# Kernel tuning notes

Hardware: AMD Instinct MI355X
Metric: run time of the kernel (lower is better)

Reference implementation:

```python
import jax, jax.numpy as jnp
import numpy as np

B, NA, OB, SD, H, GD = 512, 8, 160, 256, 4, 64
KD = GD + 1   # key_dim = gnn_output_dim + 1 = 65
NU = 32       # Multihead_Attention num_units
ED = 32       # mixing_embed_dim


def _build_edge_index():
    # fully-connected (no self loops) graph per sample, block-diagonal over batch
    idx = np.arange(NA)
    s, d = np.meshgrid(idx, idx, indexing='ij')
    mask = s != d
    s, d = s[mask], d[mask]
    offs = (np.arange(B) * NA)[:, None]
    src = (s[None, :] + offs).reshape(-1)
    dst = (d[None, :] + offs).reshape(-1)
    return jnp.asarray(np.stack([src, dst]), dtype=jnp.int32)


def setup_inputs() -> dict:
    key = jax.random.key(0)
    ks = jax.random.split(key, 16)
    p = lambda i, shape, sc=0.05: jax.random.normal(ks[i], shape, jnp.float32) * sc
    return dict(
        agent_qs=p(0, (B, NA), 1.0),
        obs=p(1, (B, NA, OB), 1.0),
        states=p(2, (B, SD), 1.0),
        edge_index=_build_edge_index(),
        W_gnn=p(3, (OB, GD)), b_gnn=jnp.zeros((GD,), jnp.float32),
        a_src=p(4, (H, GD)), a_dst=p(5, (H, GD)),
        W_h=p(6, (OB, KD * KD)), b_h=jnp.zeros((KD * KD,), jnp.float32),
        Wq=p(7, (SD, NU)), Wk=p(8, (KD, NU)),
        Wv1=p(9, (SD, ED)), bv1=jnp.zeros((ED,), jnp.float32),
        Wv2=p(10, (ED, 1)), bv2=jnp.zeros((1,), jnp.float32),
        Ww1=p(11, (SD, 64)), bw1=jnp.zeros((64,), jnp.float32),
        Ww2=p(12, (64, H)), bw2=jnp.zeros((H,), jnp.float32),
    )


def reference(agent_qs, obs, states, edge_index, W_gnn, b_gnn, a_src, a_dst,
              W_h, b_h, Wq, Wk, Wv1, bv1, Wv2, bv2, Ww1, bw1, Ww2, bw2):
    N = B * NA
    # ---- GraphPyG: GAT-style message passing with per-head edge weights ----
    x = obs.reshape(N, OB)
    h = x @ W_gnn + b_gnn                                        # [N, GD]
    src, dst = edge_index[0], edge_index[1]
    e = jax.nn.leaky_relu(h[src] @ a_src.T + h[dst] @ a_dst.T, 0.2)  # [E, H]
    m = jax.ops.segment_max(e, dst, num_segments=N)              # per-dst softmax
    ex = jnp.exp(e - m[dst])
    s = jax.ops.segment_sum(ex, dst, num_segments=N)
    alpha = ex / (s[dst] + 1e-16)                                # [E, H]
    msg = alpha[:, :, None] * h[src][:, None, :]                 # [E, H, GD]
    agg = jax.ops.segment_sum(msg, dst, num_segments=N).mean(axis=1)
    gcn = jax.nn.relu(agg).reshape(B, NA, GD)

    # ---- COO -> dense per-head weight matrices, diagonal zeroed ----
    dense = jnp.zeros((N, N, H), jnp.float32).at[src, dst].set(alpha)
    diag = jnp.arange(N)
    gnn_weight_matrics = dense.at[diag, diag].set(0.0)           # [N, N, H]

    # ---- hypernet-weighted keys (qgraph_fix branch) ----
    keys = jnp.concatenate([agent_qs[:, :, None], gcn], axis=-1)  # [B, NA, KD]
    w1 = jnp.abs(obs.reshape(-1, OB) @ W_h + b_h).reshape(-1, KD, KD)
    keys = jax.nn.elu(jnp.einsum('nk,nkj->nj', keys.reshape(-1, KD), w1))
    keys = keys.reshape(B, NA, KD)

    # ---- multihead attention mixer: query=state, key=keys, value=agent_qs ----
    d = NU // H
    q = (states @ Wq).reshape(B, 1, H, d).transpose(0, 2, 1, 3)   # [B,H,1,d]
    k = (keys @ Wk).reshape(B, NA, H, d).transpose(0, 2, 1, 3)    # [B,H,NA,d]
    scores = jnp.einsum('bhqd,bhkd->bhqk', q, k) / jnp.sqrt(jnp.float32(d))
    attn = jax.nn.softmax(scores, axis=-1)                        # [B,H,1,NA]
    out = jnp.einsum('bhqk,bk->bhq', attn, agent_qs).transpose(0, 2, 1)  # [B,1,H]

    # ---- squared head weights + state bias V ----
    head_w = (jax.nn.relu(states @ Ww1 + bw1) @ Ww2 + bw2) ** 2   # [B,H]
    q_tot = jnp.sum(out * head_w[:, None, :], axis=-1, keepdims=True)  # [B,1,1]
    v = (jax.nn.relu(states @ Wv1 + bv1) @ Wv2 + bv2)[:, :, None]      # [B,1,1]
    return (q_tot + v, attn, gnn_weight_matrics)
```

## Files before the change

### kernel.cpp

```cpp
#include <hip/hip_runtime.h>


typedef short short8v __attribute__((ext_vector_type(8)));
typedef float float4v __attribute__((ext_vector_type(4)));

#define NBATCH 512
#define NAG 8
#define OBD 160
#define SDD 256
#define NHD 4
#define GDD 64
#define NKD 65
#define NCOL 4225
#define NNODE 4096
#define NSPLIT 8
#define CPS 529
#define OUT1_OFF 512
#define OUT2_OFF 16896
#define DENSE_N4 16777216
#define NFILL 2048
#define NPREP 660
#define NZERO 260
#define WHT_BYTE_OFF 2129920
#define WS_NEED_BF16 3481984

__device__ __forceinline__ ushort f2b(float f) {
    union { float f; uint i; } x; x.f = f;
    uint r = (x.i + 0x7FFFu + ((x.i >> 16) & 1u)) >> 16;
    return (ushort)r;
}

__global__ __launch_bounds__(256) void k_pre(
    const float* __restrict__ aq, const float* __restrict__ obs,
    const float* __restrict__ Wg, const float* __restrict__ bg,
    const float* __restrict__ asrc, const float* __restrict__ adst,
    const float* __restrict__ Wh,
    float* __restrict__ kv, float* __restrict__ keys_acc,
    ushort* __restrict__ WhT, float* __restrict__ dense, int do_prep)
{
    int blk = blockIdx.x, t = threadIdx.x;

    if (blk >= NBATCH) {
        int r = blk - NBATCH;
        if (r < NPREP) {
            if (!do_prep) return;
            for (int i = r * 256 + t; i < NCOL * OBD; i += NPREP * 256) {
                int k = i / NCOL, c = i - k * NCOL;
                WhT[(size_t)c * OBD + k] = f2b(Wh[i]);
            }
        } else {
            int z4 = (r - NPREP) * 256 + t;
            ((float4v*)keys_acc)[z4] = float4v{0.f, 0.f, 0.f, 0.f};
        }
        return;
    }

    int b = blk;
    __shared__ float obs_s[NAG][OBD];
    __shared__ float h_s[NAG][GDD];
    __shared__ float u_s[NAG][NHD], v_s[NAG][NHD];
    __shared__ float al_s[NAG][NAG][NHD];
    __shared__ float c_s[NAG][NAG];

    const float* ob = obs + (size_t)b * (NAG * OBD);
    for (int u = t; u < NAG * OBD; u += 256) obs_s[u / OBD][u % OBD] = ob[u];
    __syncthreads();

    {
        int g = t & 63, i0 = t >> 6;
        float a0 = bg[g], a1 = a0;
        for (int c = 0; c < OBD; ++c) {
            float w = Wg[c * GDD + g];
            a0 += obs_s[i0][c] * w;
            a1 += obs_s[i0 + 4][c] * w;
        }
        h_s[i0][g] = a0; h_s[i0 + 4][g] = a1;
    }
    __syncthreads();

    if (t < 64) {
        int i = (t >> 2) & 7, hd = t & 3;
        const float* av = (t >= 32) ? adst : asrc;
        float a = 0.f;
        for (int g = 0; g < GDD; ++g) a += h_s[i][g] * av[hd * GDD + g];
        if (t >= 32) v_s[i][hd] = a; else u_s[i][hd] = a;
    }
    __syncthreads();

    if (t < 32) {
        int d = t >> 2, hd = t & 3;
        float e[NAG], m = -1e30f;
        for (int s = 0; s < NAG; ++s) {
            if (s == d) { e[s] = -1e30f; continue; }
            float x = u_s[s][hd] + v_s[d][hd];
            x = x > 0.f ? x : 0.2f * x;
            e[s] = x; if (x > m) m = x;
        }
        float sum = 0.f;
        for (int s = 0; s < NAG; ++s) {
            float ex = (s == d) ? 0.f : expf(e[s] - m);
            sum += ex; al_s[s][d][hd] = ex;
        }
        float inv = 1.f / (sum + 1e-16f);
        for (int s = 0; s < NAG; ++s) al_s[s][d][hd] *= inv;
    }
    __syncthreads();

    if (t < 64) {
        int s = t >> 3, d = t & 7;
        c_s[s][d] = 0.25f * (al_s[s][d][0] + al_s[s][d][1] + al_s[s][d][2] + al_s[s][d][3]);
    }
    __syncthreads();

    {
        int g = t & 63, d0 = t >> 6;
        for (int dd = d0; dd < NAG; dd += 4) {
            float a = 0.f;
            for (int s = 0; s < NAG; ++s) a += c_s[s][dd] * h_s[s][g];
            a = a > 0.f ? a : 0.f;
            kv[(size_t)(b * NAG + dd) * NKD + 1 + g] = a;
        }
    }
    if (t < NAG) kv[(size_t)(b * NAG + t) * NKD] = aq[b * NAG + t];

    {
        int s = t >> 5, pos = t & 31, d = pos >> 2, hd = pos & 3;
        float v = (d == s) ? 0.f : al_s[s][d][hd];
        dense[(size_t)(b * NAG + s) * (NNODE * NHD) + b * 32 + pos] = v;
    }
}

__global__ __launch_bounds__(256) void k_fuse_bf16(
    const float* __restrict__ obs, const ushort* __restrict__ WhT,
    const float* __restrict__ bh, const float* __restrict__ kv,
    float* __restrict__ keys_acc, float* __restrict__ dense)
{
    __shared__ float kv_s[64][NKD];
    __shared__ float ak[64][NKD];
    int t = threadIdx.x;

    if (blockIdx.x >= NSPLIT * 64) {
        int fb = blockIdx.x - NSPLIT * 64;
        size_t i = (size_t)fb * 256 + t;
        const size_t stride = (size_t)NFILL * 256;
        float4v z = {0.f, 0.f, 0.f, 0.f};
        float4v* d4 = (float4v*)dense;
        for (; i < DENSE_N4; i += stride) {
            uint off4 = (uint)i & 4095u;
            uint span4 = ((uint)(i >> 15)) << 3;
            if (off4 - span4 < 8u) continue;
            d4[i] = z;
        }
        return;
    }

    int hid = blockIdx.x;
    int ns = hid & 7, mb = hid >> 3;
    int lane = t & 63, w = t >> 6;
    int q = lane >> 4, col = lane & 15;
    int cstart = ns * CPS;
    int cend = NCOL < cstart + CPS ? NCOL : cstart + CPS;

    for (int u = t; u < 64 * NKD; u += 256) {
        ((float*)kv_s)[u] = kv[(size_t)(mb * 64) * NKD + u];
        ((float*)ak)[u] = 0.f;
    }

    int row_g = mb * 64 + w * 16 + col;
    short8v a8[5];
    #pragma unroll
    for (int ks = 0; ks < 5; ++ks) {
        const float* p = obs + (size_t)row_g * OBD + ks * 32 + q * 8;
        float4v lo = *(const float4v*)p;
        float4v hi = *(const float4v*)(p + 4);
        a8[ks] = short8v{(short)f2b(lo[0]), (short)f2b(lo[1]), (short)f2b(lo[2]), (short)f2b(lo[3]),
                         (short)f2b(hi[0]), (short)f2b(hi[1]), (short)f2b(hi[2]), (short)f2b(hi[3])};
    }
    __syncthreads();

    for (int cb = cstart; cb < cend; cb += 16) {
        int c2 = cb + col;
        uint cc = (uint)(c2 < NCOL ? c2 : NCOL - 1);
        float4v acc = {0.f, 0.f, 0.f, 0.f};
        const ushort* bp = WhT + (size_t)cc * OBD;
        #pragma unroll
        for (int ks = 0; ks < 5; ++ks) {
            short8v b8 = *(const short8v*)(bp + ks * 32 + q * 8);
            acc = __builtin_amdgcn_mfma_f32_16x16x32_bf16(a8[ks], b8, acc, 0, 0, 0);
        }
        if (c2 < cend) {
            float bias = bh[c2];
            int k2 = c2 / NKD, j = c2 - k2 * NKD;
            #pragma unroll
            for (int r = 0; r < 4; ++r) {
                int rl = w * 16 + q * 4 + r;
                ak[rl][j] += kv_s[rl][k2] * fabsf(acc[r] + bias);
            }
        }
    }
    __syncthreads();

    for (int u = t; u < 64 * NKD; u += 256)
        atomicAdd(&keys_acc[(size_t)(mb * 64) * NKD + u], ((float*)ak)[u]);
}

__global__ __launch_bounds__(256) void k_fuse_f32(
    const float* __restrict__ obs, const float* __restrict__ Wh,
    const float* __restrict__ bh, const float* __restrict__ kv,
    float* __restrict__ keys_acc, float* __restrict__ dense)
{
    __shared__ float kv_s[64][NKD];
    __shared__ float ak[64][NKD];
    int t = threadIdx.x;

    if (blockIdx.x >= NSPLIT * 64) {
        int fb = blockIdx.x - NSPLIT * 64;
        size_t i = (size_t)fb * 256 + t;
        const size_t stride = (size_t)NFILL * 256;
        float4v z = {0.f, 0.f, 0.f, 0.f};
        float4v* d4 = (float4v*)dense;
        for (; i < DENSE_N4; i += stride) {
            uint off4 = (uint)i & 4095u;
            uint span4 = ((uint)(i >> 15)) << 3;
            if (off4 - span4 < 8u) continue;
            d4[i] = z;
        }
        return;
    }

    int hid = blockIdx.x;
    int ns = hid & 7, mb = hid >> 3;
    int lane = t & 63, w = t >> 6;
    int q = lane >> 4, col = lane & 15;
    int cstart = ns * CPS;
    int cend = NCOL < cstart + CPS ? NCOL : cstart + CPS;

    for (int u = t; u < 64 * NKD; u += 256) {
        ((float*)kv_s)[u] = kv[(size_t)(mb * 64) * NKD + u];
        ((float*)ak)[u] = 0.f;
    }

    int row_g = mb * 64 + w * 16 + col;
    short8v a8[5];
    #pragma unroll
    for (int ks = 0; ks < 5; ++ks) {
        const float* p = obs + (size_t)row_g * OBD + ks * 32 + q * 8;
        float4v lo = *(const float4v*)p;
        float4v hi = *(const float4v*)(p + 4);
        a8[ks] = short8v{(short)f2b(lo[0]), (short)f2b(lo[1]), (short)f2b(lo[2]), (short)f2b(lo[3]),
                         (short)f2b(hi[0]), (short)f2b(hi[1]), (short)f2b(hi[2]), (short)f2b(hi[3])};
    }
    __syncthreads();

    for (int cb = cstart; cb < cend; cb += 16) {
        int c2 = cb + col;
        uint cc = (uint)(c2 < NCOL ? c2 : NCOL - 1);
        float4v acc = {0.f, 0.f, 0.f, 0.f};
        #pragma unroll
        for (int ks = 0; ks < 5; ++ks) {
            uint kbase = (uint)(ks * 32 + q * 8) * (uint)NCOL + cc;
            short8v b8;
            #pragma unroll
            for (int r = 0; r < 8; ++r)
                b8[r] = (short)f2b(Wh[kbase + (uint)r * (uint)NCOL]);
            acc = __builtin_amdgcn_mfma_f32_16x16x32_bf16(a8[ks], b8, acc, 0, 0, 0);
        }
        if (c2 < cend) {
            float bias = bh[c2];
            int k2 = c2 / NKD, j = c2 - k2 * NKD;
            #pragma unroll
            for (int r = 0; r < 4; ++r) {
                int rl = w * 16 + q * 4 + r;
                ak[rl][j] += kv_s[rl][k2] * fabsf(acc[r] + bias);
            }
        }
    }
    __syncthreads();

    for (int u = t; u < 64 * NKD; u += 256)
        atomicAdd(&keys_acc[(size_t)(mb * 64) * NKD + u], ((float*)ak)[u]);
}

__global__ __launch_bounds__(256) void k_attn(
    const float* __restrict__ aq, const float* __restrict__ states,
    const float* __restrict__ keys_acc,
    const float* __restrict__ Wq, const float* __restrict__ Wk,
    const float* __restrict__ Wv1, const float* __restrict__ bv1,
    const float* __restrict__ Wv2, const float* __restrict__ bv2,
    const float* __restrict__ Ww1, const float* __restrict__ bw1,
    const float* __restrict__ Ww2, const float* __restrict__ bw2,
    float* __restrict__ out)
{
    int b = blockIdx.x, t = threadIdx.x;
    __shared__ float st_s[SDD];
    __shared__ float keys_s[NAG][NKD];
    __shared__ float q_s[32], h1_s[64], hv_s[32];
    __shared__ float kp_s[NAG][32];
    __shared__ float oh_s[NHD], hw_s[NHD];

    st_s[t] = states[(size_t)b * SDD + t];
    for (int u = t; u < NAG * NKD; u += 256) {
        int n = u / NKD, j = u - NKD * n;
        float s = keys_acc[(size_t)(b * NAG + n) * NKD + j];
        keys_s[n][j] = s > 0.f ? s : (expf(s) - 1.f);
    }
    __syncthreads();

    if (t < 32) {
        float a = 0.f;
        for (int c = 0; c < SDD; ++c) a += st_s[c] * Wq[c * 32 + t];
        q_s[t] = a;
    } else if (t < 96) {
        int z = t - 32; float a = bw1[z];
        for (int c = 0; c < SDD; ++c) a += st_s[c] * Ww1[c * 64 + z];
        h1_s[z] = fmaxf(a, 0.f);
    } else if (t < 128) {
        int z = t - 96; float a = bv1[z];
        for (int c = 0; c < SDD; ++c) a += st_s[c] * Wv1[c * 32 + z];
        hv_s[z] = fmaxf(a, 0.f);
    }
    __syncthreads();

    {
        int i = t >> 5, u = t & 31;
        float a = 0.f;
        for (int j = 0; j < NKD; ++j) a += keys_s[i][j] * Wk[j * 32 + u];
        kp_s[i][u] = a;
    }
    __syncthreads();

    if (t < NHD) {
        int hd = t;
        float sc[NAG], m = -1e30f;
        for (int i = 0; i < NAG; ++i) {
            float a = 0.f;
            for (int dd = 0; dd < 8; ++dd) a += q_s[hd * 8 + dd] * kp_s[i][hd * 8 + dd];
            a *= 0.35355339059327373f;
            sc[i] = a; if (a > m) m = a;
        }
        float sum = 0.f;
        for (int i = 0; i < NAG; ++i) { sc[i] = expf(sc[i] - m); sum += sc[i]; }
        float inv = 1.f / sum, oh = 0.f;
        for (int i = 0; i < NAG; ++i) {
            float at = sc[i] * inv;
            out[OUT1_OFF + (size_t)(b * NHD + hd) * NAG + i] = at;
            oh += at * aq[b * NAG + i];
        }
        oh_s[hd] = oh;
        float hw = bw2[hd];
        for (int z = 0; z < 64; ++z) hw += h1_s[z] * Ww2[z * NHD + hd];
        hw_s[hd] = hw * hw;
    }
    __syncthreads();

    if (t == 0) {
        float v = bv2[0];
        for (int z = 0; z < 32; ++z) v += hv_s[z] * Wv2[z];
        float qt = 0.f;
        for (int hd = 0; hd < NHD; ++hd) qt += oh_s[hd] * hw_s[hd];
        out[b] = qt + v;
    }
}

extern "C" void kernel_launch(void* const* d_in, const int* in_sizes, int n_in,
                              void* d_out, int out_size, void* d_ws, size_t ws_size,
                              hipStream_t stream) {
    const float* aq   = (const float*)d_in[0];
    const float* obs  = (const float*)d_in[1];
    const float* st   = (const float*)d_in[2];
    const float* Wg   = (const float*)d_in[4];
    const float* bg   = (const float*)d_in[5];
    const float* asrc = (const float*)d_in[6];
    const float* adst = (const float*)d_in[7];
    const float* Wh   = (const float*)d_in[8];
    const float* bh   = (const float*)d_in[9];
    const float* Wq_  = (const float*)d_in[10];
    const float* Wk_  = (const float*)d_in[11];
    const float* Wv1  = (const float*)d_in[12];
    const float* bv1  = (const float*)d_in[13];
    const float* Wv2  = (const float*)d_in[14];
    const float* bv2  = (const float*)d_in[15];
    const float* Ww1  = (const float*)d_in[16];
    const float* bw1  = (const float*)d_in[17];
    const float* Ww2  = (const float*)d_in[18];
    const float* bw2  = (const float*)d_in[19];
    float* out = (float*)d_out;
    float* dense = out + OUT2_OFF;

    float*  kv       = (float*)d_ws;
    float*  keys_acc = kv + (size_t)NNODE * NKD;
    ushort* WhT      = (ushort*)((char*)d_ws + WHT_BYTE_OFF);
    int bf16path = (ws_size >= (size_t)WS_NEED_BF16) ? 1 : 0;

    k_pre<<<NBATCH + NPREP + NZERO, 256, 0, stream>>>(
        aq, obs, Wg, bg, asrc, adst, Wh, kv, keys_acc, WhT, dense, bf16path);

    if (bf16path)
        k_fuse_bf16<<<NSPLIT * 64 + NFILL, 256, 0, stream>>>(obs, WhT, bh, kv, keys_acc, dense);
    else
        k_fuse_f32<<<NSPLIT * 64 + NFILL, 256, 0, stream>>>(obs, Wh, bh, kv, keys_acc, dense);

    k_attn<<<NBATCH, 256, 0, stream>>>(aq, st, keys_acc, Wq_, Wk_, Wv1, bv1, Wv2, bv2,
                                       Ww1, bw1, Ww2, bw2, out);
}
```

Baseline: 115.1 us.

## Reuse B fragments across four row tiles and write per-split partial sums

```diff
diff --git a/kernel.cpp b/kernel.cpp
--- a/kernel.cpp
+++ b/kernel.cpp
@@ -21,8 +21,7 @@
 #define NFILL 2048
 #define NPREP 660
 #define NZERO 260
-#define WHT_BYTE_OFF 2129920
-#define WS_NEED_BF16 3481984
+#define KVN ((size_t)NNODE * NKD)
 
 __device__ __forceinline__ ushort f2b(float f) {
     union { float f; uint i; } x; x.f = f;
@@ -35,7 +34,7 @@
     const float* __restrict__ Wg, const float* __restrict__ bg,
     const float* __restrict__ asrc, const float* __restrict__ adst,
     const float* __restrict__ Wh,
-    float* __restrict__ kv, float* __restrict__ keys_acc,
+    float* __restrict__ kv, float* __restrict__ zptr,
     ushort* __restrict__ WhT, float* __restrict__ dense, int do_prep)
 {
     int blk = blockIdx.x, t = threadIdx.x;
@@ -50,7 +49,7 @@
             }
         } else {
             int z4 = (r - NPREP) * 256 + t;
-            ((float4v*)keys_acc)[z4] = float4v{0.f, 0.f, 0.f, 0.f};
+            ((float4v*)zptr)[z4] = float4v{0.f, 0.f, 0.f, 0.f};
         }
         return;
     }
@@ -130,13 +129,13 @@
     }
 }
 
-__global__ __launch_bounds__(256) void k_fuse_bf16(
-    const float* __restrict__ obs, const ushort* __restrict__ WhT,
-    const float* __restrict__ bh, const float* __restrict__ kv,
-    float* __restrict__ keys_acc, float* __restrict__ dense)
+template<int MODE>
+__global__ __launch_bounds__(256) void k_fuse(
+    const float* __restrict__ obs, const float* __restrict__ Wh,
+    const ushort* __restrict__ WhT, const float* __restrict__ bh,
+    const float* __restrict__ kv, float* __restrict__ outacc,
+    float* __restrict__ dense)
 {
-    __shared__ float kv_s[64][NKD];
-    __shared__ float ak[64][NKD];
     int t = threadIdx.x;
 
     if (blockIdx.x >= NSPLIT * 64) {
@@ -154,8 +153,10 @@
         return;
     }
 
-    int hid = blockIdx.x;
-    int ns = hid & 7, mb = hid >> 3;
+    __shared__ float kv_s[64][NKD];
+    __shared__ float ak[64][NKD];
+
+    int ns = blockIdx.x & 7, mb = blockIdx.x >> 3;
     int lane = t & 63, w = t >> 6;
     int q = lane >> 4, col = lane & 15;
     int cstart = ns * CPS;
@@ -166,124 +167,74 @@
         ((float*)ak)[u] = 0.f;
     }
 
-    int row_g = mb * 64 + w * 16 + col;
-    short8v a8[5];
+    short8v a8[4][5];
     #pragma unroll
-    for (int ks = 0; ks < 5; ++ks) {
-        const float* p = obs + (size_t)row_g * OBD + ks * 32 + q * 8;
-        float4v lo = *(const float4v*)p;
-        float4v hi = *(const float4v*)(p + 4);
-        a8[ks] = short8v{(short)f2b(lo[0]), (short)f2b(lo[1]), (short)f2b(lo[2]), (short)f2b(lo[3]),
-                         (short)f2b(hi[0]), (short)f2b(hi[1]), (short)f2b(hi[2]), (short)f2b(hi[3])};
-    }
-    __syncthreads();
-
-    for (int cb = cstart; cb < cend; cb += 16) {
+    for (int rt = 0; rt < 4; ++rt) {
+        int row_g = mb * 64 + rt * 16 + col;
+        #pragma unroll
+        for (int ks = 0; ks < 5; ++ks) {
+            const float* p = obs + (size_t)row_g * OBD + ks * 32 + q * 8;
+            float4v lo = *(const float4v*)p;
+            float4v hi = *(const float4v*)(p + 4);
+            a8[rt][ks] = short8v{(short)f2b(lo[0]), (short)f2b(lo[1]), (short)f2b(lo[2]), (short)f2b(lo[3]),
+                                 (short)f2b(hi[0]), (short)f2b(hi[1]), (short)f2b(hi[2]), (short)f2b(hi[3])};
+        }
+    }
+    __syncthreads();
+
+    for (int cb = cstart + w * 16; cb < cend; cb += 64) {
         int c2 = cb + col;
         uint cc = (uint)(c2 < NCOL ? c2 : NCOL - 1);
-        float4v acc = {0.f, 0.f, 0.f, 0.f};
-        const ushort* bp = WhT + (size_t)cc * OBD;
+        short8v b8[5];
+        if (MODE == 2) {
+            #pragma unroll
+            for (int ks = 0; ks < 5; ++ks) {
+                uint kbase = (uint)(ks * 32 + q * 8) * (uint)NCOL + cc;
+                #pragma unroll
+                for (int r = 0; r < 8; ++r)
+                    b8[ks][r] = (short)f2b(Wh[kbase + (uint)r * (uint)NCOL]);
+            }
+        } else {
+            const ushort* bp = WhT + (size_t)cc * OBD;
+            #pragma unroll
+            for (int ks = 0; ks < 5; ++ks)
+                b8[ks] = *(const short8v*)(bp + ks * 32 + q * 8);
+        }
+        float4v acc0 = {0,0,0,0}, acc1 = {0,0,0,0}, acc2 = {0,0,0,0}, acc3 = {0,0,0,0};
         #pragma unroll
         for (int ks = 0; ks < 5; ++ks) {
-            short8v b8 = *(const short8v*)(bp + ks * 32 + q * 8);
-            acc = __builtin_amdgcn_mfma_f32_16x16x32_bf16(a8[ks], b8, acc, 0, 0, 0);
+            acc0 = __builtin_amdgcn_mfma_f32_16x16x32_bf16(a8[0][ks], b8[ks], acc0, 0, 0, 0);
+            acc1 = __builtin_amdgcn_mfma_f32_16x16x32_bf16(a8[1][ks], b8[ks], acc1, 0, 0, 0);
+            acc2 = __builtin_amdgcn_mfma_f32_16x16x32_bf16(a8[2][ks], b8[ks], acc2, 0, 0, 0);
+            acc3 = __builtin_amdgcn_mfma_f32_16x16x32_bf16(a8[3][ks], b8[ks], acc3, 0, 0, 0);
         }
         if (c2 < cend) {
             float bias = bh[c2];
             int k2 = c2 / NKD, j = c2 - k2 * NKD;
             #pragma unroll
             for (int r = 0; r < 4; ++r) {
-                int rl = w * 16 + q * 4 + r;
-                ak[rl][j] += kv_s[rl][k2] * fabsf(acc[r] + bias);
+                int rb = q * 4 + r;
+                atomicAdd(&ak[rb     ][j], kv_s[rb     ][k2] * fabsf(acc0[r] + bias));
+                atomicAdd(&ak[rb + 16][j], kv_s[rb + 16][k2] * fabsf(acc1[r] + bias));
+                atomicAdd(&ak[rb + 32][j], kv_s[rb + 32][k2] * fabsf(acc2[r] + bias));
+                atomicAdd(&ak[rb + 48][j], kv_s[rb + 48][k2] * fabsf(acc3[r] + bias));
             }
         }
     }
     __syncthreads();
 
-    for (int u = t; u < 64 * NKD; u += 256)
-        atomicAdd(&keys_acc[(size_t)(mb * 64) * NKD + u], ((float*)ak)[u]);
-}
-
-__global__ __launch_bounds__(256) void k_fuse_f32(
-    const float* __restrict__ obs, const float* __restrict__ Wh,
-    const float* __restrict__ bh, const float* __restrict__ kv,
-    float* __restrict__ keys_acc, float* __restrict__ dense)
-{
-    __shared__ float kv_s[64][NKD];
-    __shared__ float ak[64][NKD];
-    int t = threadIdx.x;
-
-    if (blockIdx.x >= NSPLIT * 64) {
-        int fb = blockIdx.x - NSPLIT * 64;
-        size_t i = (size_t)fb * 256 + t;
-        const size_t stride = (size_t)NFILL * 256;
-        float4v z = {0.f, 0.f, 0.f, 0.f};
-        float4v* d4 = (float4v*)dense;
-        for (; i < DENSE_N4; i += stride) {
-            uint off4 = (uint)i & 4095u;
-            uint span4 = ((uint)(i >> 15)) << 3;
-            if (off4 - span4 < 8u) continue;
-            d4[i] = z;
-        }
-        return;
-    }
-
-    int hid = blockIdx.x;
-    int ns = hid & 7, mb = hid >> 3;
-    int lane = t & 63, w = t >> 6;
-    int q = lane >> 4, col = lane & 15;
-    int cstart = ns * CPS;
-    int cend = NCOL < cstart + CPS ? NCOL : cstart + CPS;
-
-    for (int u = t; u < 64 * NKD; u += 256) {
-        ((float*)kv_s)[u] = kv[(size_t)(mb * 64) * NKD + u];
-        ((float*)ak)[u] = 0.f;
-    }
-
-    int row_g = mb * 64 + w * 16 + col;
-    short8v a8[5];
-    #pragma unroll
-    for (int ks = 0; ks < 5; ++ks) {
-        const float* p = obs + (size_t)row_g * OBD + ks * 32 + q * 8;
-        float4v lo = *(const float4v*)p;
-        float4v hi = *(const float4v*)(p + 4);
-        a8[ks] = short8v{(short)f2b(lo[0]), (short)f2b(lo[1]), (short)f2b(lo[2]), (short)f2b(lo[3]),
-                         (short)f2b(hi[0]), (short)f2b(hi[1]), (short)f2b(hi[2]), (short)f2b(hi[3])};
-    }
-    __syncthreads();
-
-    for (int cb = cstart; cb < cend; cb += 16) {
-        int c2 = cb + col;
-        uint cc = (uint)(c2 < NCOL ? c2 : NCOL - 1);
-        float4v acc = {0.f, 0.f, 0.f, 0.f};
-        #pragma unroll
-        for (int ks = 0; ks < 5; ++ks) {
-            uint kbase = (uint)(ks * 32 + q * 8) * (uint)NCOL + cc;
-            short8v b8;
-            #pragma unroll
-            for (int r = 0; r < 8; ++r)
-                b8[r] = (short)f2b(Wh[kbase + (uint)r * (uint)NCOL]);
-            acc = __builtin_amdgcn_mfma_f32_16x16x32_bf16(a8[ks], b8, acc, 0, 0, 0);
-        }
-        if (c2 < cend) {
-            float bias = bh[c2];
-            int k2 = c2 / NKD, j = c2 - k2 * NKD;
-            #pragma unroll
-            for (int r = 0; r < 4; ++r) {
-                int rl = w * 16 + q * 4 + r;
-                ak[rl][j] += kv_s[rl][k2] * fabsf(acc[r] + bias);
-            }
-        }
-    }
-    __syncthreads();
-
-    for (int u = t; u < 64 * NKD; u += 256)
-        atomicAdd(&keys_acc[(size_t)(mb * 64) * NKD + u], ((float*)ak)[u]);
+    if (MODE == 0) {
+        float* dst = outacc + ((size_t)ns * NNODE + mb * 64) * NKD;
+        for (int u = t; u < 64 * NKD; u += 256) dst[u] = ((float*)ak)[u];
+    } else {
+        for (int u = t; u < 64 * NKD; u += 256)
+            atomicAdd(&outacc[(size_t)(mb * 64) * NKD + u], ((float*)ak)[u]);
+    }
 }
 
 __global__ __launch_bounds__(256) void k_attn(
     const float* __restrict__ aq, const float* __restrict__ states,
-    const float* __restrict__ keys_acc,
+    const float* __restrict__ keysrc, int nparts,
     const float* __restrict__ Wq, const float* __restrict__ Wk,
     const float* __restrict__ Wv1, const float* __restrict__ bv1,
     const float* __restrict__ Wv2, const float* __restrict__ bv2,
@@ -301,7 +252,14 @@
     st_s[t] = states[(size_t)b * SDD + t];
     for (int u = t; u < NAG * NKD; u += 256) {
         int n = u / NKD, j = u - NKD * n;
-        float s = keys_acc[(size_t)(b * NAG + n) * NKD + j];
+        size_t base = (size_t)(b * NAG + n) * NKD + j;
+        float s;
+        if (nparts) {
+            s = 0.f;
+            for (int p = 0; p < nparts; ++p) s += keysrc[(size_t)p * KVN + base];
+        } else {
+            s = keysrc[base];
+        }
         keys_s[n][j] = s > 0.f ? s : (expf(s) - 1.f);
     }
     __syncthreads();
@@ -387,19 +345,36 @@
     float* out = (float*)d_out;
     float* dense = out + OUT2_OFF;
 
-    float*  kv       = (float*)d_ws;
-    float*  keys_acc = kv + (size_t)NNODE * NKD;
-    ushort* WhT      = (ushort*)((char*)d_ws + WHT_BYTE_OFF);
-    int bf16path = (ws_size >= (size_t)WS_NEED_BF16) ? 1 : 0;
+    float* kv = (float*)d_ws;
+    const size_t NEED_PART = (1 + NSPLIT) * KVN * 4 + (size_t)NCOL * OBD * 2;
+    const size_t NEED_WHT  = 2 * KVN * 4 + (size_t)NCOL * OBD * 2;
+
+    int mode, nparts;
+    float* outacc;
+    ushort* WhT = (ushort*)d_ws;
+    if (ws_size >= NEED_PART) {
+        mode = 0; nparts = NSPLIT;
+        outacc = kv + KVN;
+        WhT = (ushort*)((char*)d_ws + (1 + NSPLIT) * KVN * 4);
+    } else if (ws_size >= NEED_WHT) {
+        mode = 1; nparts = 0;
+        outacc = kv + KVN;
+        WhT = (ushort*)((char*)d_ws + 2 * KVN * 4);
+    } else {
+        mode = 2; nparts = 0;
+        outacc = kv + KVN;
+    }
 
     k_pre<<<NBATCH + NPREP + NZERO, 256, 0, stream>>>(
-        aq, obs, Wg, bg, asrc, adst, Wh, kv, keys_acc, WhT, dense, bf16path);
-
-    if (bf16path)
-        k_fuse_bf16<<<NSPLIT * 64 + NFILL, 256, 0, stream>>>(obs, WhT, bh, kv, keys_acc, dense);
+        aq, obs, Wg, bg, asrc, adst, Wh, kv, outacc, WhT, dense, mode != 2);
+
+    if (mode == 0)
+        k_fuse<0><<<NSPLIT * 64 + NFILL, 256, 0, stream>>>(obs, Wh, WhT, bh, kv, outacc, dense);
+    else if (mode == 1)
+        k_fuse<1><<<NSPLIT * 64 + NFILL, 256, 0, stream>>>(obs, Wh, WhT, bh, kv, outacc, dense);
     else
-        k_fuse_f32<<<NSPLIT * 64 + NFILL, 256, 0, stream>>>(obs, Wh, bh, kv, keys_acc, dense);
-
-    k_attn<<<NBATCH, 256, 0, stream>>>(aq, st, keys_acc, Wq_, Wk_, Wv1, bv1, Wv2, bv2,
-                                       Ww1, bw1, Ww2, bw2, out);
-}
+        k_fuse<2><<<NSPLIT * 64 + NFILL, 256, 0, stream>>>(obs, Wh, WhT, bh, kv, outacc, dense);
+
+    k_attn<<<NBATCH, 256, 0, stream>>>(aq, st, outacc, nparts, Wq_, Wk_, Wv1, bv1,
+                                       Wv2, bv2, Ww1, bw1, Ww2, bw2, out);
+}
```

Result: slower. 181.7 us (+57.9%).

## Reorder hypernet weights by output column to reduce keys in registers

Applied to the files above, without the earlier changes.

```diff
diff --git a/kernel.cpp b/kernel.cpp
--- a/kernel.cpp
+++ b/kernel.cpp
@@ -13,16 +13,20 @@
 #define NKD 65
 #define NCOL 4225
 #define NNODE 4096
-#define NSPLIT 8
-#define CPS 529
 #define OUT1_OFF 512
 #define OUT2_OFF 16896
 #define DENSE_N4 16777216
 #define NFILL 2048
 #define NPREP 660
 #define NZERO 260
-#define WHT_BYTE_OFF 2129920
-#define WS_NEED_BF16 3481984
+#define NSPLIT_R 13
+#define NHYP (NSPLIT_R * 64)
+#define PCOL 5200
+#define NSPLIT_F 8
+#define CPS 529
+#define KVN ((size_t)NNODE * NKD)
+#define WHT_OFF (2 * KVN * 4)
+#define WS_NEED (WHT_OFF + (size_t)PCOL * OBD * 2)
 
 __device__ __forceinline__ ushort f2b(float f) {
     union { float f; uint i; } x; x.f = f;
@@ -36,7 +40,7 @@
     const float* __restrict__ asrc, const float* __restrict__ adst,
     const float* __restrict__ Wh,
     float* __restrict__ kv, float* __restrict__ keys_acc,
-    ushort* __restrict__ WhT, float* __restrict__ dense, int do_prep)
+    ushort* __restrict__ WhTr, float* __restrict__ dense, int do_prep)
 {
     int blk = blockIdx.x, t = threadIdx.x;
 
@@ -44,9 +48,10 @@
         int r = blk - NBATCH;
         if (r < NPREP) {
             if (!do_prep) return;
-            for (int i = r * 256 + t; i < NCOL * OBD; i += NPREP * 256) {
-                int k = i / NCOL, c = i - k * NCOL;
-                WhT[(size_t)c * OBD + k] = f2b(Wh[i]);
+            for (int i = r * 256 + t; i < PCOL * OBD; i += NPREP * 256) {
+                int p = i / OBD, kk = i - p * OBD;
+                int j = p / 80, k = p - j * 80;
+                WhTr[i] = (k < NKD) ? f2b(Wh[(size_t)kk * NCOL + k * NKD + j]) : (ushort)0;
             }
         } else {
             int z4 = (r - NPREP) * 256 + t;
@@ -130,17 +135,15 @@
     }
 }
 
-__global__ __launch_bounds__(256) void k_fuse_bf16(
-    const float* __restrict__ obs, const ushort* __restrict__ WhT,
+__global__ __launch_bounds__(256) void k_fuse_r(
+    const float* __restrict__ obs, const ushort* __restrict__ WhTr,
     const float* __restrict__ bh, const float* __restrict__ kv,
     float* __restrict__ keys_acc, float* __restrict__ dense)
 {
-    __shared__ float kv_s[64][NKD];
-    __shared__ float ak[64][NKD];
     int t = threadIdx.x;
 
-    if (blockIdx.x >= NSPLIT * 64) {
-        int fb = blockIdx.x - NSPLIT * 64;
+    if (blockIdx.x >= NHYP) {
+        int fb = blockIdx.x - NHYP;
         size_t i = (size_t)fb * 256 + t;
         const size_t stride = (size_t)NFILL * 256;
         float4v z = {0.f, 0.f, 0.f, 0.f};
@@ -154,16 +157,19 @@
         return;
     }
 
-    int hid = blockIdx.x;
-    int ns = hid & 7, mb = hid >> 3;
+    __shared__ float kv_s[64][NKD];
+    __shared__ float bh_s[5][80];
+
+    int sid = blockIdx.x % NSPLIT_R, mb = blockIdx.x / NSPLIT_R;
     int lane = t & 63, w = t >> 6;
     int q = lane >> 4, col = lane & 15;
-    int cstart = ns * CPS;
-    int cend = NCOL < cstart + CPS ? NCOL : cstart + CPS;
-
-    for (int u = t; u < 64 * NKD; u += 256) {
+    int j0 = sid * 5;
+
+    for (int u = t; u < 64 * NKD; u += 256)
         ((float*)kv_s)[u] = kv[(size_t)(mb * 64) * NKD + u];
-        ((float*)ak)[u] = 0.f;
+    for (int u = t; u < 400; u += 256) {
+        int jj = u / 80, k = u - jj * 80;
+        bh_s[jj][k] = (k < NKD) ? bh[k * NKD + j0 + jj] : 0.f;
     }
 
     int row_g = mb * 64 + w * 16 + col;
@@ -178,30 +184,38 @@
     }
     __syncthreads();
 
-    for (int cb = cstart; cb < cend; cb += 16) {
-        int c2 = cb + col;
-        uint cc = (uint)(c2 < NCOL ? c2 : NCOL - 1);
-        float4v acc = {0.f, 0.f, 0.f, 0.f};
-        const ushort* bp = WhT + (size_t)cc * OBD;
+    int rl = w * 16 + q * 4;
+    for (int jj = 0; jj < 5; ++jj) {
+        float sacc[4] = {0.f, 0.f, 0.f, 0.f};
         #pragma unroll
-        for (int ks = 0; ks < 5; ++ks) {
-            short8v b8 = *(const short8v*)(bp + ks * 32 + q * 8);
-            acc = __builtin_amdgcn_mfma_f32_16x16x32_bf16(a8[ks], b8, acc, 0, 0, 0);
-        }
-        if (c2 < cend) {
-            float bias = bh[c2];
-            int k2 = c2 / NKD, j = c2 - k2 * NKD;
+        for (int c5 = 0; c5 < 5; ++c5) {
+            int k = c5 * 16 + col;
+            int p = sid * 400 + jj * 80 + k;
+            const ushort* bp = WhTr + (size_t)p * OBD;
+            float4v acc = {0.f, 0.f, 0.f, 0.f};
+            #pragma unroll
+            for (int ks = 0; ks < 5; ++ks) {
+                short8v b8 = *(const short8v*)(bp + ks * 32 + q * 8);
+                acc = __builtin_amdgcn_mfma_f32_16x16x32_bf16(a8[ks], b8, acc, 0, 0, 0);
+            }
+            float bias = bh_s[jj][k];
             #pragma unroll
             for (int r = 0; r < 4; ++r) {
-                int rl = w * 16 + q * 4 + r;
-                ak[rl][j] += kv_s[rl][k2] * fabsf(acc[r] + bias);
+                float kw = (k < NKD) ? kv_s[rl + r][k] : 0.f;
+                sacc[r] += kw * fabsf(acc[r] + bias);
             }
         }
-    }
-    __syncthreads();
-
-    for (int u = t; u < 64 * NKD; u += 256)
-        atomicAdd(&keys_acc[(size_t)(mb * 64) * NKD + u], ((float*)ak)[u]);
+        #pragma unroll
+        for (int r = 0; r < 4; ++r) {
+            float v = sacc[r];
+            v += __shfl_xor(v, 1);
+            v += __shfl_xor(v, 2);
+            v += __shfl_xor(v, 4);
+            v += __shfl_xor(v, 8);
+            if (col == 0)
+                atomicAdd(&keys_acc[(size_t)(mb * 64 + rl + r) * NKD + j0 + jj], v);
+        }
+    }
 }
 
 __global__ __launch_bounds__(256) void k_fuse_f32(
@@ -213,8 +227,8 @@
     __shared__ float ak[64][NKD];
     int t = threadIdx.x;
 
-    if (blockIdx.x >= NSPLIT * 64) {
-        int fb = blockIdx.x - NSPLIT * 64;
+    if (blockIdx.x >= NSPLIT_F * 64) {
+        int fb = blockIdx.x - NSPLIT_F * 64;
         size_t i = (size_t)fb * 256 + t;
         const size_t stride = (size_t)NFILL * 256;
         float4v z = {0.f, 0.f, 0.f, 0.f};
@@ -228,8 +242,7 @@
         return;
     }
 
-    int hid = blockIdx.x;
-    int ns = hid & 7, mb = hid >> 3;
+    int ns = blockIdx.x & 7, mb = blockIdx.x >> 3;
     int lane = t & 63, w = t >> 6;
     int q = lane >> 4, col = lane & 15;
     int cstart = ns * CPS;
@@ -388,17 +401,17 @@
     float* dense = out + OUT2_OFF;
 
     float*  kv       = (float*)d_ws;
-    float*  keys_acc = kv + (size_t)NNODE * NKD;
-    ushort* WhT      = (ushort*)((char*)d_ws + WHT_BYTE_OFF);
-    int bf16path = (ws_size >= (size_t)WS_NEED_BF16) ? 1 : 0;
+    float*  keys_acc = kv + KVN;
+    ushort* WhTr     = (ushort*)((char*)d_ws + WHT_OFF);
+    int rpath = (ws_size >= WS_NEED) ? 1 : 0;
 
     k_pre<<<NBATCH + NPREP + NZERO, 256, 0, stream>>>(
-        aq, obs, Wg, bg, asrc, adst, Wh, kv, keys_acc, WhT, dense, bf16path);
-
-    if (bf16path)
-        k_fuse_bf16<<<NSPLIT * 64 + NFILL, 256, 0, stream>>>(obs, WhT, bh, kv, keys_acc, dense);
+        aq, obs, Wg, bg, asrc, adst, Wh, kv, keys_acc, WhTr, dense, rpath);
+
+    if (rpath)
+        k_fuse_r<<<NHYP + NFILL, 256, 0, stream>>>(obs, WhTr, bh, kv, keys_acc, dense);
     else
-        k_fuse_f32<<<NSPLIT * 64 + NFILL, 256, 0, stream>>>(obs, Wh, bh, kv, keys_acc, dense);
+        k_fuse_f32<<<NSPLIT_F * 64 + NFILL, 256, 0, stream>>>(obs, Wh, bh, kv, keys_acc, dense);
 
     k_attn<<<NBATCH, 256, 0, stream>>>(aq, st, keys_acc, Wq_, Wk_, Wv1, bv1, Wv2, bv2,
                                        Ww1, bw1, Ww2, bw2, out);
```

Measured after the change: 96.35 us. -16.3%, faster.
